# Kernel optimization log

Measured on AMD Instinct MI355X. Metric: run time of the kernel, lower is better.

## Reference

```python
import jax, jax.numpy as jnp
import numpy as np

N = 50000      # nodes / stations
E = 600000     # edges
IN = 16        # in_channels
ED = 8         # edge_dim
HID = 128      # hidden
H = 4          # heads
C = HID // H   # 32 per-head channels
EMB = HID // 2 # station embedding dim
FEAT = HID - EMB
SLOPE = 0.2    # GATv2 LeakyReLU negative slope


def setup_inputs() -> dict:
    key = jax.random.key(0)
    ks = jax.random.split(key, 32)
    r = lambda i, shape, s=0.05: (jax.random.normal(ks[i], shape, jnp.float32) * s)
    inp = {
        "x": jax.random.normal(ks[0], (N, IN), jnp.float32),
        "node_idx": jax.random.randint(ks[1], (N,), 0, N),
        "edge_index": jax.random.randint(ks[2], (2, E), 0, N),
        "edge_attr": jax.random.normal(ks[3], (E, ED), jnp.float32),
        # params
        "emb": r(4, (N, EMB)),
        "W_in": r(5, (IN, FEAT)), "b_in": jnp.zeros((FEAT,), jnp.float32),
        # conv1 (GATv2: lin_l, lin_r, lin_edge, att, out bias)
        "Wl1": r(6, (HID, HID)), "bl1": jnp.zeros((HID,), jnp.float32),
        "Wr1": r(7, (HID, HID)), "br1": jnp.zeros((HID,), jnp.float32),
        "We1": r(8, (ED, HID)),  "be1": jnp.zeros((HID,), jnp.float32),
        "att1": r(9, (H, C)),    "bo1": jnp.zeros((HID,), jnp.float32),
        # conv2
        "Wl2": r(10, (HID, HID)), "bl2": jnp.zeros((HID,), jnp.float32),
        "Wr2": r(11, (HID, HID)), "br2": jnp.zeros((HID,), jnp.float32),
        "We2": r(12, (ED, HID)),  "be2": jnp.zeros((HID,), jnp.float32),
        "att2": r(13, (H, C)),    "bo2": jnp.zeros((HID,), jnp.float32),
        # layer norms
        "g1": jnp.ones((HID,), jnp.float32), "beta1": jnp.zeros((HID,), jnp.float32),
        "g2": jnp.ones((HID,), jnp.float32), "beta2": jnp.zeros((HID,), jnp.float32),
        # output head
        "W_out": r(14, (HID, 1)), "b_out": jnp.zeros((1,), jnp.float32),
    }
    return inp


def _gatv2(x, src, dst, ea, Wl, bl, Wr, br, We, be, att, bo):
    # x: [N,HID] -> per-head projections [N,H,C]
    xl = (x @ Wl + bl).reshape(-1, H, C)   # source transform
    xr = (x @ Wr + br).reshape(-1, H, C)   # target transform
    ee = (ea @ We + be).reshape(-1, H, C)  # edge transform [E,H,C]
    s = jax.nn.leaky_relu(xl[src] + xr[dst] + ee, SLOPE)  # [E,H,C]
    logit = jnp.einsum('ehc,hc->eh', s, att)              # [E,H]
    # segment softmax over destination node
    amax = jax.lax.stop_gradient(jax.ops.segment_max(logit, dst, num_segments=N))
    amax = jnp.where(jnp.isfinite(amax), amax, 0.0)
    ex = jnp.exp(logit - amax[dst])
    den = jax.ops.segment_sum(ex, dst, num_segments=N)
    alpha = ex / den[dst]                                  # [E,H]
    out = jax.ops.segment_sum(xl[src] * alpha[..., None], dst, num_segments=N)
    return out.reshape(-1, HID) + bo


def _ln(x, g, b):
    mu = x.mean(-1, keepdims=True)
    v = ((x - mu) ** 2).mean(-1, keepdims=True)
    return (x - mu) * jax.lax.rsqrt(v + 1e-5) * g + b


def reference(x, node_idx, edge_index, edge_attr, emb, W_in, b_in,
              Wl1, bl1, Wr1, br1, We1, be1, att1, bo1,
              Wl2, bl2, Wr2, br2, We2, be2, att2, bo2,
              g1, beta1, g2, beta2, W_out, b_out):
    src, dst = edge_index[0], edge_index[1]
    feat = jax.nn.relu(x @ W_in + b_in)                       # [N,FEAT]
    z = jnp.concatenate([feat, emb[node_idx]], axis=-1)       # [N,HID]
    h = jax.nn.relu(_gatv2(z, src, dst, edge_attr, Wl1, bl1, Wr1, br1, We1, be1, att1, bo1))
    z = _ln(z + h, g1, beta1)
    h = jax.nn.relu(_gatv2(z, src, dst, edge_attr, Wl2, bl2, Wr2, br2, We2, be2, att2, bo2))
    z = _ln(z + h, g2, beta2)
    return (z @ W_out + b_out).squeeze(-1)                    # [N]
```

## Files before the change

kernel.cpp:

```cpp
#include <hip/hip_runtime.h>
#include <hip/hip_bf16.h>

#define NN 50000
#define NE 600000
#define IND 16
#define EDD 8
#define HIDD 128
#define NH 4
#define CC 32
#define EMBD 64
#define FEATD 64
#define NB_SCAN ((NN + 255) / 256)
#define FILLB ((NE + 255) / 256)
#define BZB (NN / 16)
#define WPB 256
#define PRMF 896

typedef __hip_bfloat16 bf16;
typedef __attribute__((ext_vector_type(8))) short bshort8;
typedef __attribute__((ext_vector_type(4))) float floatx4;
typedef __attribute__((ext_vector_type(2))) float f32x2;

__device__ __forceinline__ unsigned short f2bu(float f) {
    unsigned int u = __float_as_uint(f);
    u += 0x7fffu + ((u >> 16) & 1u);
    return (unsigned short)(u >> 16);
}

#if defined(__has_builtin)
#if __has_builtin(__builtin_amdgcn_fdot2_f32_bf16)
#define HAS_DOT2BF 1
#endif
#endif
#ifndef HAS_DOT2BF
#define HAS_DOT2BF 0
#endif

#if HAS_DOT2BF
typedef __attribute__((ext_vector_type(2))) __bf16 bfx2;
__device__ __forceinline__ float dot2bf(unsigned int a, unsigned int b, float c) {
    return __builtin_amdgcn_fdot2_f32_bf16(__builtin_bit_cast(bfx2, a),
                                           __builtin_bit_cast(bfx2, b), c, false);
}
#else
__device__ __forceinline__ float dot2bf(unsigned int a, unsigned int b, float c) {
    float a0 = __uint_as_float(a << 16), a1 = __uint_as_float(a & 0xffff0000u);
    float b0 = __uint_as_float(b << 16), b1 = __uint_as_float(b & 0xffff0000u);
    return __builtin_fmaf(a1, b1, __builtin_fmaf(a0, b0, c));
}
#endif

template <bool F32>
__device__ __forceinline__ float LD(const void* p, long long i) {
    if constexpr (F32) return ((const float*)p)[i];
    else return __bfloat162float(((const bf16*)p)[i]);
}

__device__ __forceinline__ bool is_f32(const int* cnt) { return *cnt > 8; }

__global__ void k_detinit(const unsigned short* __restrict__ x, int nhalf,
                          int* __restrict__ cnt, int* __restrict__ deg,
                          int* __restrict__ dcnt) {
    if (blockIdx.x == 0) {
        __shared__ int red[256];
        int hits = 0;
        for (int i = threadIdx.x; i < nhalf; i += 256)
            if ((x[i] & 0x7F80u) == 0x7F80u) hits++;
        red[threadIdx.x] = hits;
        __syncthreads();
        for (int o = 128; o; o >>= 1) {
            if (threadIdx.x < o) red[threadIdx.x] += red[threadIdx.x + o];
            __syncthreads();
        }
        if (threadIdx.x == 0) *cnt = red[0];
    } else {
        int gid = (blockIdx.x - 1) * 256 + threadIdx.x;
        if (gid < NN) deg[gid] = 0;
        if (blockIdx.x == 1 && threadIdx.x < 80) dcnt[threadIdx.x] = 0;
    }
}

__global__ void k_hist(const int* __restrict__ ei, int* __restrict__ deg, int* __restrict__ rank) {
    int e = blockIdx.x * blockDim.x + threadIdx.x;
    if (e < NE) rank[e] = atomicAdd(&deg[ei[NE + e]], 1);
}

__global__ void k_scan12(const int* __restrict__ deg, int* __restrict__ off0,
                         int* __restrict__ bsum, int* __restrict__ dcnt,
                         int* __restrict__ dbase, int* __restrict__ rankd) {
    __shared__ int tile[256];
    __shared__ int lh[64];
    __shared__ int lbase[64];
    __shared__ int d2[64];
    __shared__ int ticket;
    int t = threadIdx.x;
    int gid = blockIdx.x * 256 + t;
    if (t < 64) lh[t] = 0;
    __syncthreads();
    int v = (gid < NN) ? deg[gid] : 0;
    int b = 63 - min(v, 63);
    int lr = 0;
    if (gid < NN) lr = atomicAdd(&lh[b], 1);
    tile[t] = v;
    __syncthreads();
    if (t < 64) lbase[t] = lh[t] ? atomicAdd(&dcnt[t], lh[t]) : 0;
    #pragma unroll
    for (int o = 1; o < 256; o <<= 1) {
        int u = (t >= o) ? tile[t - o] : 0;
        __syncthreads();
        tile[t] += u;
        __syncthreads();
    }
    if (gid < NN) {
        off0[gid] = tile[t] - v;
        rankd[gid] = lbase[b] + lr;
    }
    if (t == 255) atomicExch(&bsum[blockIdx.x], tile[255]);
    __syncthreads();
    if (t == 0) ticket = atomicAdd(&dcnt[64], 1);
    __syncthreads();
    if (ticket != NB_SCAN - 1) return;
    int v2 = (t < NB_SCAN) ? atomicAdd(&bsum[t], 0) : 0;
    int dv = (t < 64) ? atomicAdd(&dcnt[t], 0) : 0;
    tile[t] = v2;
    if (t < 64) d2[t] = dv;
    __syncthreads();
    #pragma unroll
    for (int o = 1; o < 256; o <<= 1) {
        int u = (t >= o) ? tile[t - o] : 0;
        __syncthreads();
        tile[t] += u;
        __syncthreads();
    }
    #pragma unroll
    for (int o = 1; o < 64; o <<= 1) {
        int u = (t >= o && t < 64) ? d2[t - o] : 0;
        __syncthreads();
        if (t < 64) d2[t] += u;
        __syncthreads();
    }
    if (t < NB_SCAN) bsum[t] = tile[t] - v2;
    if (t < 64) dbase[t] = d2[t] - dv;
}

template <bool F32>
__device__ void prep_impl(const int* __restrict__ off0, const int* __restrict__ bsum,
                          const int* __restrict__ deg, const int* __restrict__ rankd,
                          const int* __restrict__ dbase, int* __restrict__ perm,
                          int* __restrict__ offF,
                          const int* __restrict__ ei, const int* __restrict__ rank,
                          int* __restrict__ esrc, uint4* __restrict__ ea8, const void* ea,
                          const void* x, const int* __restrict__ node_idx, const void* emb,
                          const void* W_in, const void* b_in, bf16* __restrict__ zb,
                          const void* Wl1, const void* bl1, const void* Wr1, const void* br1,
                          const void* Wl2, const void* bl2, const void* Wr2, const void* br2,
                          bf16* __restrict__ wbT, float* __restrict__ bias,
                          const void* We1, const void* att1, const void* be1, const void* bo1,
                          const void* g1, const void* beta1,
                          const void* We2, const void* att2, const void* be2, const void* bo2,
                          const void* g2, const void* beta2,
                          const void* Wo, const void* bout,
                          unsigned int* __restrict__ wep, float* __restrict__ prm) {
    int b = blockIdx.x;
    int t = threadIdx.x;
    if (b < NB_SCAN) {
        int gid = b * 256 + t;
        if (gid < NN) {
            offF[gid] = off0[gid] + bsum[b];
            int bk = 63 - min(deg[gid], 63);
            perm[dbase[bk] + rankd[gid]] = gid;
        }
        if (gid == 0) offF[NN] = NE;
    } else if (b < NB_SCAN + FILLB) {
        int e = (b - NB_SCAN) * 256 + t;
        if (e >= NE) return;
        if (e < 16) {
            esrc[NE + e] = 0;
            uint4 z; z.x = 0; z.y = 0; z.z = 0; z.w = 0;
            ea8[NE + e] = z;
        }
        int dst = ei[NE + e];
        int slot = off0[dst] + bsum[dst >> 8] + rank[e];
        esrc[slot] = ei[e];
        uint4 v;
        if constexpr (F32) {
            const float4* ef = (const float4*)ea;
            float4 f0 = ef[2 * e], f1 = ef[2 * e + 1];
            v.x = (unsigned int)f2bu(f0.x) | ((unsigned int)f2bu(f0.y) << 16);
            v.y = (unsigned int)f2bu(f0.z) | ((unsigned int)f2bu(f0.w) << 16);
            v.z = (unsigned int)f2bu(f1.x) | ((unsigned int)f2bu(f1.y) << 16);
            v.w = (unsigned int)f2bu(f1.z) | ((unsigned int)f2bu(f1.w) << 16);
        } else {
            v = ((const uint4*)ea)[e];
        }
        ea8[slot] = v;
    } else if (b < NB_SCAN + FILLB + BZB) {
        int nb = (b - NB_SCAN - FILLB) * 16 + (t >> 7) * 8;
        int t7 = t & 127;
        if (t7 < FEATD) {
            float w[IND];
            #pragma unroll
            for (int k = 0; k < IND; k++) w[k] = LD<F32>(W_in, k * FEATD + t7);
            float bi = LD<F32>(b_in, t7);
            #pragma unroll 2
            for (int nd = 0; nd < 8; nd++) {
                int n = nb + nd;
                float acc = bi;
                #pragma unroll
                for (int k = 0; k < IND; k++)
                    acc += LD<F32>(x, (long long)n * IND + k) * w[k];
                zb[n * HIDD + t7] = __float2bfloat16(fmaxf(acc, 0.f));
            }
        } else {
            #pragma unroll 2
            for (int nd = 0; nd < 8; nd++) {
                int n = nb + nd;
                zb[n * HIDD + t7] = __float2bfloat16(
                    LD<F32>(emb, (long long)node_idx[n] * EMBD + (t7 - FEATD)));
            }
        }
    } else if (b < NB_SCAN + FILLB + BZB + WPB) {
        int bid2 = (b - NB_SCAN - FILLB - BZB) * 2 + (t >> 7);
        int layer = bid2 >> 8;
        int n2 = bid2 & 255;
        int t7 = t & 127;
        const void* W = layer ? (n2 < HIDD ? Wl2 : Wr2) : (n2 < HIDD ? Wl1 : Wr1);
        const void* bb = layer ? (n2 < HIDD ? bl2 : br2) : (n2 < HIDD ? bl1 : br1);
        int nn = n2 & (HIDD - 1);
        wbT[(layer * 256 + n2) * HIDD + t7] = __float2bfloat16(LD<F32>(W, t7 * HIDD + nn));
        if (t7 == 0) bias[layer * 256 + n2] = LD<F32>(bb, nn);
    } else {
        int layer = b - (NB_SCAN + FILLB + BZB + WPB);
        const void* We = layer ? We2 : We1;
        const void* att = layer ? att2 : att1;
        const void* be = layer ? be2 : be1;
        const void* bo = layer ? bo2 : bo1;
        const void* g  = layer ? g2 : g1;
        const void* bt = layer ? beta2 : beta1;
        if (t < 128) {
            int lane5 = t >> 2, j = t & 3, c0 = lane5 * 4;
            #pragma unroll
            for (int p = 0; p < 4; p++) {
                unsigned int lo_ = f2bu(LD<F32>(We, (2 * p) * HIDD + c0 + j));
                unsigned int hi_ = f2bu(LD<F32>(We, (2 * p + 1) * HIDD + c0 + j));
                wep[layer * 512 + lane5 * 16 + p * 4 + j] = lo_ | (hi_ << 16);
            }
        } else {
            int t2 = t - 128;
            float* Pp = prm + layer * PRMF;
            Pp[t2]        = LD<F32>(att, t2) * 1.4426950408889634f;
            Pp[128 + t2]  = LD<F32>(be, t2);
            Pp[256 + t2]  = LD<F32>(bo, t2);
            Pp[384 + t2]  = LD<F32>(g, t2);
            Pp[512 + t2]  = LD<F32>(bt, t2);
            if (layer) {
                Pp[640 + t2] = LD<F32>(Wo, t2);
                if (t2 == 0) Pp[768] = LD<F32>(bout, 0);
            }
        }
    }
}
__global__ void k_prep(const int* cnt, const int* off0, const int* bsum, const int* deg,
                       const int* rankd, const int* dbase, int* perm, int* offF,
                       const int* ei, const int* rank, int* esrc, uint4* ea8, const void* ea,
                       const void* x, const int* node_idx, const void* emb,
                       const void* W_in, const void* b_in, bf16* zb,
                       const void* Wl1, const void* bl1, const void* Wr1, const void* br1,
                       const void* Wl2, const void* bl2, const void* Wr2, const void* br2,
                       bf16* wbT, float* bias,
                       const void* We1, const void* att1, const void* be1, const void* bo1,
                       const void* g1, const void* beta1,
                       const void* We2, const void* att2, const void* be2, const void* bo2,
                       const void* g2, const void* beta2,
                       const void* Wo, const void* bout,
                       unsigned int* wep, float* prm) {
    if (is_f32(cnt))
        prep_impl<true>(off0, bsum, deg, rankd, dbase, perm, offF, ei, rank, esrc, ea8, ea,
                        x, node_idx, emb, W_in, b_in, zb, Wl1, bl1, Wr1, br1,
                        Wl2, bl2, Wr2, br2, wbT, bias, We1, att1, be1, bo1, g1, beta1,
                        We2, att2, be2, bo2, g2, beta2, Wo, bout, wep, prm);
    else
        prep_impl<false>(off0, bsum, deg, rankd, dbase, perm, offF, ei, rank, esrc, ea8, ea,
                         x, node_idx, emb, W_in, b_in, zb, Wl1, bl1, Wr1, br1,
                         Wl2, bl2, Wr2, br2, wbT, bias, We1, att1, be1, bo1, g1, beta1,
                         We2, att2, be2, bo2, g2, beta2, Wo, bout, wep, prm);
}

__global__ __launch_bounds__(256) void k_projmm(const bf16* __restrict__ zb,
                                                const bf16* __restrict__ wbT,
                                                const float* __restrict__ bias,
                                                bf16* __restrict__ xl, bf16* __restrict__ xr) {
    int wave = threadIdx.x >> 6, lane = threadIdx.x & 63;
    int n0 = wave * 64;
    int l15 = lane & 15, q = lane >> 4;
    bshort8 afr[4][4];
    #pragma unroll
    for (int j = 0; j < 4; j++)
        #pragma unroll
        for (int s = 0; s < 4; s++)
            afr[j][s] = *(const bshort8*)(wbT + ((n0 + j * 16 + l15) << 7) + s * 32 + q * 8);
    float4 bias4[4];
    #pragma unroll
    for (int j = 0; j < 4; j++) bias4[j] = *(const float4*)(bias + n0 + j * 16 + q * 4);
    bf16* dst = (n0 < HIDD) ? xl : xr;
    int cbase = (n0 & (HIDD - 1)) + q * 4;
    int nodeBase = blockIdx.x * 64;
    #pragma unroll
    for (int mt = 0; mt < 4; mt++) {
        int node = nodeBase + mt * 16 + l15;
        const bf16* brow = zb + (node << 7) + q * 8;
        bshort8 bfrag[4];
        #pragma unroll
        for (int s = 0; s < 4; s++) bfrag[s] = *(const bshort8*)(brow + s * 32);
        floatx4 acc0 = {0.f, 0.f, 0.f, 0.f}, acc1 = acc0, acc2 = acc0, acc3 = acc0;
        #pragma unroll
        for (int s = 0; s < 4; s++) {
            acc0 = __builtin_amdgcn_mfma_f32_16x16x32_bf16(afr[0][s], bfrag[s], acc0, 0, 0, 0);
            acc1 = __builtin_amdgcn_mfma_f32_16x16x32_bf16(afr[1][s], bfrag[s], acc1, 0, 0, 0);
            acc2 = __builtin_amdgcn_mfma_f32_16x16x32_bf16(afr[2][s], bfrag[s], acc2, 0, 0, 0);
            acc3 = __builtin_amdgcn_mfma_f32_16x16x32_bf16(afr[3][s], bfrag[s], acc3, 0, 0, 0);
        }
        if (node < NN) {
            floatx4 accs[4] = {acc0, acc1, acc2, acc3};
            #pragma unroll
            for (int j = 0; j < 4; j++) {
                float4 bv = bias4[j];
                uint2 pk;
                pk.x = (unsigned int)f2bu(accs[j][0] + bv.x) |
                       ((unsigned int)f2bu(accs[j][1] + bv.y) << 16);
                pk.y = (unsigned int)f2bu(accs[j][2] + bv.z) |
                       ((unsigned int)f2bu(accs[j][3] + bv.w) << 16);
                *(uint2*)(dst + (node << 7) + cbase + j * 16) = pk;
            }
        }
    }
}

__device__ __forceinline__ void edge_body(uint4 eu, uint2 xu, const unsigned int (*wp)[4],
                                          const float* base, const f32x2* at2,
                                          float mask, f32x2* acc, float& den) {
    f32x2 xv0, xv1;
    xv0.x = __uint_as_float(xu.x << 16); xv0.y = __uint_as_float(xu.x & 0xffff0000u);
    xv1.x = __uint_as_float(xu.y << 16); xv1.y = __uint_as_float(xu.y & 0xffff0000u);
    f32x2 e01, e23;
    {
        float c0 = base[0];
        c0 = dot2bf(eu.x, wp[0][0], c0);
        c0 = dot2bf(eu.y, wp[1][0], c0);
        c0 = dot2bf(eu.z, wp[2][0], c0);
        c0 = dot2bf(eu.w, wp[3][0], c0);
        float c1 = base[1];
        c1 = dot2bf(eu.x, wp[0][1], c1);
        c1 = dot2bf(eu.y, wp[1][1], c1);
        c1 = dot2bf(eu.z, wp[2][1], c1);
        c1 = dot2bf(eu.w, wp[3][1], c1);
        e01.x = c0; e01.y = c1;
        float c2 = base[2];
        c2 = dot2bf(eu.x, wp[0][2], c2);
        c2 = dot2bf(eu.y, wp[1][2], c2);
        c2 = dot2bf(eu.z, wp[2][2], c2);
        c2 = dot2bf(eu.w, wp[3][2], c2);
        float c3 = base[3];
        c3 = dot2bf(eu.x, wp[0][3], c3);
        c3 = dot2bf(eu.y, wp[1][3], c3);
        c3 = dot2bf(eu.z, wp[2][3], c3);
        c3 = dot2bf(eu.w, wp[3][3], c3);
        e23.x = c2; e23.y = c3;
    }
    f32x2 s0 = xv0 + e01;
    f32x2 s1 = xv1 + e23;
    s0 = __builtin_elementwise_max(s0, s0 * 0.2f);
    s1 = __builtin_elementwise_max(s1, s1 * 0.2f);
    f32x2 lsv = s0 * at2[0] + s1 * at2[1];
    float ls = lsv.x + lsv.y;
    ls += __shfl_xor(ls, 1);
    ls += __shfl_xor(ls, 2);
    ls += __shfl_xor(ls, 4);
    float ex = exp2f(ls) * mask;
    acc[0] += ex * xv0;
    acc[1] += ex * xv1;
    den += ex;
}

template <bool LAST>
__device__ __forceinline__ void gat_impl(const int* __restrict__ perm,
                         const int* __restrict__ off, const int* __restrict__ esrc,
                         const uint4* __restrict__ ea8,
                         const unsigned int* __restrict__ wep,
                         const float* __restrict__ P,
                         const bf16* __restrict__ xl, const bf16* __restrict__ xr,
                         bf16* __restrict__ zb, void* out, bool f32out) {
    int wave = threadIdx.x >> 6;
    int half = (threadIdx.x >> 5) & 1;
    int lane5 = threadIdx.x & 31;
    int n = perm[blockIdx.x * 8 + wave * 2 + half];
    int c0 = lane5 << 2;
    unsigned int wp[4][4];
    {
        const uint4* w4 = (const uint4*)(wep + lane5 * 16);
        uint4 wa = w4[0], wb = w4[1], wc = w4[2], wd = w4[3];
        wp[0][0] = wa.x; wp[0][1] = wa.y; wp[0][2] = wa.z; wp[0][3] = wa.w;
        wp[1][0] = wb.x; wp[1][1] = wb.y; wp[1][2] = wb.z; wp[1][3] = wb.w;
        wp[2][0] = wc.x; wp[2][1] = wc.y; wp[2][2] = wc.z; wp[2][3] = wc.w;
        wp[3][0] = wd.x; wp[3][1] = wd.y; wp[3][2] = wd.z; wp[3][3] = wd.w;
    }
    float4 atv = *(const float4*)(P + c0);
    f32x2 at2[2];
    at2[0].x = atv.x; at2[0].y = atv.y;
    at2[1].x = atv.z; at2[1].y = atv.w;
    float4 bev = *(const float4*)(P + 128 + c0);
    uint2 xru = *(const uint2*)(xr + (n << 7) + c0);
    float base[4];
    base[0] = bev.x + __uint_as_float(xru.x << 16);
    base[1] = bev.y + __uint_as_float(xru.x & 0xffff0000u);
    base[2] = bev.z + __uint_as_float(xru.y << 16);
    base[3] = bev.w + __uint_as_float(xru.y & 0xffff0000u);
    int lo = off[n], hi = off[n + 1];
    f32x2 accA[2] = {{0.f, 0.f}, {0.f, 0.f}}, accB[2] = {{0.f, 0.f}, {0.f, 0.f}};
    float denA = 0.f, denB = 0.f;
    if (lo < hi) {
        int sA = esrc[lo],      sB = esrc[lo + 1];
        int snA = esrc[lo + 2], snB = esrc[lo + 3];
        int s2A = esrc[lo + 4], s2B = esrc[lo + 5];
        int s6A = esrc[lo + 6], s6B = esrc[lo + 7];
        int s8A = esrc[lo + 8], s8B = esrc[lo + 9];
        uint4 eA = ea8[lo],      eB = ea8[lo + 1];
        uint4 enA = ea8[lo + 2], enB = ea8[lo + 3];
        uint4 e2A = ea8[lo + 4], e2B = ea8[lo + 5];
        uint2 xA  = *(const uint2*)(xl + (sA << 7) + c0);
        uint2 xB  = *(const uint2*)(xl + (sB << 7) + c0);
        uint2 xnA = *(const uint2*)(xl + (snA << 7) + c0);
        uint2 xnB = *(const uint2*)(xl + (snB << 7) + c0);
        uint2 x2A = *(const uint2*)(xl + (s2A << 7) + c0);
        uint2 x2B = *(const uint2*)(xl + (s2B << 7) + c0);
        for (int i = lo; i < hi; i += 2) {
            uint2 x3A = *(const uint2*)(xl + (s6A << 7) + c0);
            uint2 x3B = *(const uint2*)(xl + (s6B << 7) + c0);
            uint4 e3A = ea8[i + 6], e3B = ea8[i + 7];
            int s10A = esrc[i + 10], s10B = esrc[i + 11];
            edge_body(eA, xA, wp, base, at2, 1.f, accA, denA);
            float mB = (i + 1 < hi) ? 1.f : 0.f;
            edge_body(eB, xB, wp, base, at2, mB, accB, denB);
            eA = enA; enA = e2A; e2A = e3A;
            eB = enB; enB = e2B; e2B = e3B;
            xA = xnA; xnA = x2A; x2A = x3A;
            xB = xnB; xnB = x2B; x2B = x3B;
            s6A = s8A; s8A = s10A;
            s6B = s8B; s8B = s10B;
        }
        accA[0] += accB[0];
        accA[1] += accB[1];
        denA += denB;
    }
    float inv = (denA > 0.f) ? 1.0f / denA : 0.f;
    uint2 zu = *(const uint2*)(zb + (n << 7) + c0);
    float zv[4];
    zv[0] = __uint_as_float(zu.x << 16);
    zv[1] = __uint_as_float(zu.x & 0xffff0000u);
    zv[2] = __uint_as_float(zu.y << 16);
    zv[3] = __uint_as_float(zu.y & 0xffff0000u);
    float accf[4] = {accA[0].x, accA[0].y, accA[1].x, accA[1].y};
    float4 bo4 = *(const float4*)(P + 256 + c0);
    float bov[4] = {bo4.x, bo4.y, bo4.z, bo4.w};
    float v[4];
    float s = 0.f;
    #pragma unroll
    for (int j = 0; j < 4; j++) {
        float hv = fmaxf(accf[j] * inv + bov[j], 0.f);
        v[j] = zv[j] + hv;
        s += v[j];
    }
    #pragma unroll
    for (int m = 16; m; m >>= 1) s += __shfl_xor(s, m);
    float mu = s * (1.f / HIDD);
    float s2v = 0.f;
    float dv[4];
    #pragma unroll
    for (int j = 0; j < 4; j++) { dv[j] = v[j] - mu; s2v += dv[j] * dv[j]; }
    #pragma unroll
    for (int m = 16; m; m >>= 1) s2v += __shfl_xor(s2v, m);
    float rs = rsqrtf(s2v * (1.f / HIDD) + 1e-5f);
    float4 g4 = *(const float4*)(P + 384 + c0);
    float4 bt4 = *(const float4*)(P + 512 + c0);
    float gv[4] = {g4.x, g4.y, g4.z, g4.w};
    float btv[4] = {bt4.x, bt4.y, bt4.z, bt4.w};
    float o[4];
    #pragma unroll
    for (int j = 0; j < 4; j++)
        o[j] = dv[j] * rs * gv[j] + btv[j];
    if constexpr (!LAST) {
        uint2 pk;
        pk.x = (unsigned int)f2bu(o[0]) | ((unsigned int)f2bu(o[1]) << 16);
        pk.y = (unsigned int)f2bu(o[2]) | ((unsigned int)f2bu(o[3]) << 16);
        *(uint2*)(zb + (n << 7) + c0) = pk;
    } else {
        float4 wo4 = *(const float4*)(P + 640 + c0);
        float wov[4] = {wo4.x, wo4.y, wo4.z, wo4.w};
        float po = 0.f;
        #pragma unroll
        for (int j = 0; j < 4; j++) po += o[j] * wov[j];
        #pragma unroll
        for (int m = 16; m; m >>= 1) po += __shfl_xor(po, m);
        if (lane5 == 0) {
            float r = po + P[768];
            if (f32out) ((float*)out)[n] = r;
            else        ((bf16*)out)[n] = __float2bfloat16(r);
        }
    }
}
__global__ void k_gat(const int* perm, const int* off, const int* esrc,
                      const uint4* ea8, const unsigned int* wep, const float* prm,
                      const bf16* xl, const bf16* xr, bf16* zb) {
    gat_impl<false>(perm, off, esrc, ea8, wep, prm, xl, xr, zb, nullptr, false);
}
__global__ void k_gat_last(const int* cnt, const int* perm, const int* off, const int* esrc,
                           const uint4* ea8, const unsigned int* wep, const float* prm,
                           const bf16* xl, const bf16* xr, bf16* zb, void* out) {
    gat_impl<true>(perm, off, esrc, ea8, wep, prm, xl, xr, zb, out, is_f32(cnt));
}

extern "C" void kernel_launch(void* const* d_in, const int* in_sizes, int n_in,
                              void* d_out, int out_size, void* d_ws, size_t ws_size,
                              hipStream_t stream) {
    const void* x        = d_in[0];
    const int*  node_idx = (const int*)d_in[1];
    const int*  ei       = (const int*)d_in[2];
    const void* ea       = d_in[3];
    const void* emb      = d_in[4];
    const void* W_in     = d_in[5];
    const void* b_in     = d_in[6];
    const void* Wl1 = d_in[7];  const void* bl1 = d_in[8];
    const void* Wr1 = d_in[9];  const void* br1 = d_in[10];
    const void* We1 = d_in[11]; const void* be1 = d_in[12];
    const void* att1 = d_in[13]; const void* bo1 = d_in[14];
    const void* Wl2 = d_in[15]; const void* bl2 = d_in[16];
    const void* Wr2 = d_in[17]; const void* br2 = d_in[18];
    const void* We2 = d_in[19]; const void* be2 = d_in[20];
    const void* att2 = d_in[21]; const void* bo2 = d_in[22];
    const void* g1 = d_in[23]; const void* beta1 = d_in[24];
    const void* g2 = d_in[25]; const void* beta2 = d_in[26];
    const void* W_out = d_in[27]; const void* b_out = d_in[28];

    int*   cnt   = (int*)d_ws;
    uint4* ea8   = (uint4*)((char*)d_ws + 256);
    bf16*  zb    = (bf16*)(ea8 + NE + 16);
    bf16*  xl    = zb + NN * HIDD;
    bf16*  xr    = xl + NN * HIDD;
    bf16*  wbT   = xr + NN * HIDD;
    float* bias  = (float*)(wbT + 2 * 256 * HIDD);
    unsigned int* wep = (unsigned int*)(bias + 512);
    float* prm   = (float*)(wep + 1024);
    int*   off0  = (int*)(prm + 2 * PRMF);
    int*   offF  = off0 + NN + 1;
    int*   deg   = offF + NN + 1;
    int*   rank  = deg + NN;
    int*   rankd = rank + NE;
    int*   perm  = rankd + NN;
    int*   esrc  = perm + NN;
    int*   bsum  = esrc + NE + 16;
    int*   dcnt  = bsum + 256;
    int*   dbase = dcnt + 80;

    int nhalf = in_sizes[0] < 16384 ? in_sizes[0] : 16384;
    k_detinit<<<NB_SCAN + 1, 256, 0, stream>>>((const unsigned short*)x, nhalf, cnt, deg, dcnt);
    k_hist<<<FILLB, 256, 0, stream>>>(ei, deg, rank);
    k_scan12<<<NB_SCAN, 256, 0, stream>>>(deg, off0, bsum, dcnt, dbase, rankd);
    k_prep<<<NB_SCAN + FILLB + BZB + WPB + 2, 256, 0, stream>>>(
        cnt, off0, bsum, deg, rankd, dbase, perm, offF, ei, rank, esrc, ea8, ea,
        x, node_idx, emb, W_in, b_in, zb,
        Wl1, bl1, Wr1, br1, Wl2, bl2, Wr2, br2, wbT, bias,
        We1, att1, be1, bo1, g1, beta1,
        We2, att2, be2, bo2, g2, beta2,
        W_out, b_out, wep, prm);

    k_projmm<<<(NN + 63) / 64, 256, 0, stream>>>(zb, wbT, bias, xl, xr);
    k_gat<<<NN / 8, 256, 0, stream>>>(perm, offF, esrc, ea8, wep, prm, xl, xr, zb);

    k_projmm<<<(NN + 63) / 64, 256, 0, stream>>>(zb, wbT + 256 * HIDD, bias + 256, xl, xr);
    k_gat_last<<<NN / 8, 256, 0, stream>>>(cnt, perm, offF, esrc, ea8, wep + 512, prm + PRMF,
                                           xl, xr, zb, d_out);
}
```

Before: 349.7 us.

## Split CSR edge fill into index scatter plus gather pass fused with projection

The prep kernel now scatters only the original edge id into each CSR slot. A new kernel then gathers the source index and edge attributes per slot, so the attribute writes become coalesced reads-by-index instead of a random scatter. That gather pass shares one launch with the first projection GEMM. The GAT edge loop's prefetch depth for source indices and xl rows is also reduced, trading latency hiding for fewer registers. The extra pass adds one more read and write of esrc.

```diff
diff --git a/kernel.cpp b/kernel.cpp
--- a/kernel.cpp
+++ b/kernel.cpp
@@ -14,6 +14,7 @@
 #define FILLB ((NE + 255) / 256)
 #define BZB (NN / 16)
 #define WPB 256
+#define PJB ((NN + 63) / 64)
 #define PRMF 896
 
 typedef __hip_bfloat16 bf16;
@@ -149,7 +150,7 @@
                           const int* __restrict__ dbase, int* __restrict__ perm,
                           int* __restrict__ offF,
                           const int* __restrict__ ei, const int* __restrict__ rank,
-                          int* __restrict__ esrc, uint4* __restrict__ ea8, const void* ea,
+                          int* __restrict__ esrc,
                           const void* x, const int* __restrict__ node_idx, const void* emb,
                           const void* W_in, const void* b_in, bf16* __restrict__ zb,
                           const void* Wl1, const void* bl1, const void* Wr1, const void* br1,
@@ -174,26 +175,9 @@
     } else if (b < NB_SCAN + FILLB) {
         int e = (b - NB_SCAN) * 256 + t;
         if (e >= NE) return;
-        if (e < 16) {
-            esrc[NE + e] = 0;
-            uint4 z; z.x = 0; z.y = 0; z.z = 0; z.w = 0;
-            ea8[NE + e] = z;
-        }
         int dst = ei[NE + e];
         int slot = off0[dst] + bsum[dst >> 8] + rank[e];
-        esrc[slot] = ei[e];
-        uint4 v;
-        if constexpr (F32) {
-            const float4* ef = (const float4*)ea;
-            float4 f0 = ef[2 * e], f1 = ef[2 * e + 1];
-            v.x = (unsigned int)f2bu(f0.x) | ((unsigned int)f2bu(f0.y) << 16);
-            v.y = (unsigned int)f2bu(f0.z) | ((unsigned int)f2bu(f0.w) << 16);
-            v.z = (unsigned int)f2bu(f1.x) | ((unsigned int)f2bu(f1.y) << 16);
-            v.w = (unsigned int)f2bu(f1.z) | ((unsigned int)f2bu(f1.w) << 16);
-        } else {
-            v = ((const uint4*)ea)[e];
-        }
-        ea8[slot] = v;
+        esrc[slot] = e;
     } else if (b < NB_SCAN + FILLB + BZB) {
         int nb = (b - NB_SCAN - FILLB) * 16 + (t >> 7) * 8;
         int t7 = t & 127;
@@ -262,7 +246,7 @@
 }
 __global__ void k_prep(const int* cnt, const int* off0, const int* bsum, const int* deg,
                        const int* rankd, const int* dbase, int* perm, int* offF,
-                       const int* ei, const int* rank, int* esrc, uint4* ea8, const void* ea,
+                       const int* ei, const int* rank, int* esrc,
                        const void* x, const int* node_idx, const void* emb,
                        const void* W_in, const void* b_in, bf16* zb,
                        const void* Wl1, const void* bl1, const void* Wr1, const void* br1,
@@ -275,21 +259,21 @@
                        const void* Wo, const void* bout,
                        unsigned int* wep, float* prm) {
     if (is_f32(cnt))
-        prep_impl<true>(off0, bsum, deg, rankd, dbase, perm, offF, ei, rank, esrc, ea8, ea,
+        prep_impl<true>(off0, bsum, deg, rankd, dbase, perm, offF, ei, rank, esrc,
                         x, node_idx, emb, W_in, b_in, zb, Wl1, bl1, Wr1, br1,
                         Wl2, bl2, Wr2, br2, wbT, bias, We1, att1, be1, bo1, g1, beta1,
                         We2, att2, be2, bo2, g2, beta2, Wo, bout, wep, prm);
     else
-        prep_impl<false>(off0, bsum, deg, rankd, dbase, perm, offF, ei, rank, esrc, ea8, ea,
+        prep_impl<false>(off0, bsum, deg, rankd, dbase, perm, offF, ei, rank, esrc,
                          x, node_idx, emb, W_in, b_in, zb, Wl1, bl1, Wr1, br1,
                          Wl2, bl2, Wr2, br2, wbT, bias, We1, att1, be1, bo1, g1, beta1,
                          We2, att2, be2, bo2, g2, beta2, Wo, bout, wep, prm);
 }
 
-__global__ __launch_bounds__(256) void k_projmm(const bf16* __restrict__ zb,
-                                                const bf16* __restrict__ wbT,
-                                                const float* __restrict__ bias,
-                                                bf16* __restrict__ xl, bf16* __restrict__ xr) {
+__device__ __forceinline__ void projmm_body(int vb, const bf16* __restrict__ zb,
+                                            const bf16* __restrict__ wbT,
+                                            const float* __restrict__ bias,
+                                            bf16* __restrict__ xl, bf16* __restrict__ xr) {
     int wave = threadIdx.x >> 6, lane = threadIdx.x & 63;
     int n0 = wave * 64;
     int l15 = lane & 15, q = lane >> 4;
@@ -304,7 +288,7 @@
     for (int j = 0; j < 4; j++) bias4[j] = *(const float4*)(bias + n0 + j * 16 + q * 4);
     bf16* dst = (n0 < HIDD) ? xl : xr;
     int cbase = (n0 & (HIDD - 1)) + q * 4;
-    int nodeBase = blockIdx.x * 64;
+    int nodeBase = vb * 64;
     #pragma unroll
     for (int mt = 0; mt < 4; mt++) {
         int node = nodeBase + mt * 16 + l15;
@@ -333,6 +317,49 @@
                 *(uint2*)(dst + (node << 7) + cbase + j * 16) = pk;
             }
         }
+    }
+}
+__global__ __launch_bounds__(256) void k_projmm(const bf16* __restrict__ zb,
+                                                const bf16* __restrict__ wbT,
+                                                const float* __restrict__ bias,
+                                                bf16* __restrict__ xl, bf16* __restrict__ xr) {
+    projmm_body(blockIdx.x, zb, wbT, bias, xl, xr);
+}
+
+template <bool F32>
+__device__ void f2_impl(int* __restrict__ esrc, uint4* __restrict__ ea8,
+                        const int* __restrict__ ei, const void* ea) {
+    int slot = blockIdx.x * 256 + threadIdx.x;
+    if (slot >= NE) return;
+    if (slot < 16) {
+        esrc[NE + slot] = 0;
+        uint4 z; z.x = 0; z.y = 0; z.z = 0; z.w = 0;
+        ea8[NE + slot] = z;
+    }
+    int e = esrc[slot];
+    esrc[slot] = ei[e];
+    uint4 v;
+    if constexpr (F32) {
+        const float4* ef = (const float4*)ea;
+        float4 f0 = ef[2 * e], f1 = ef[2 * e + 1];
+        v.x = (unsigned int)f2bu(f0.x) | ((unsigned int)f2bu(f0.y) << 16);
+        v.y = (unsigned int)f2bu(f0.z) | ((unsigned int)f2bu(f0.w) << 16);
+        v.z = (unsigned int)f2bu(f1.x) | ((unsigned int)f2bu(f1.y) << 16);
+        v.w = (unsigned int)f2bu(f1.z) | ((unsigned int)f2bu(f1.w) << 16);
+    } else {
+        v = ((const uint4*)ea)[e];
+    }
+    ea8[slot] = v;
+}
+__global__ __launch_bounds__(256) void k_f2pm(const int* cnt, int* esrc, uint4* ea8,
+                                              const int* ei, const void* ea,
+                                              const bf16* zb, const bf16* wbT,
+                                              const float* bias, bf16* xl, bf16* xr) {
+    if (blockIdx.x < FILLB) {
+        if (is_f32(cnt)) f2_impl<true>(esrc, ea8, ei, ea);
+        else             f2_impl<false>(esrc, ea8, ei, ea);
+    } else {
+        projmm_body(blockIdx.x - FILLB, zb, wbT, bias, xl, xr);
     }
 }
 
@@ -420,33 +447,28 @@
     float denA = 0.f, denB = 0.f;
     if (lo < hi) {
         int sA = esrc[lo],      sB = esrc[lo + 1];
+        uint4 eA = ea8[lo],     eB = ea8[lo + 1];
         int snA = esrc[lo + 2], snB = esrc[lo + 3];
+        uint4 enA = ea8[lo + 2], enB = ea8[lo + 3];
         int s2A = esrc[lo + 4], s2B = esrc[lo + 5];
-        int s6A = esrc[lo + 6], s6B = esrc[lo + 7];
-        int s8A = esrc[lo + 8], s8B = esrc[lo + 9];
-        uint4 eA = ea8[lo],      eB = ea8[lo + 1];
-        uint4 enA = ea8[lo + 2], enB = ea8[lo + 3];
         uint4 e2A = ea8[lo + 4], e2B = ea8[lo + 5];
-        uint2 xA  = *(const uint2*)(xl + (sA << 7) + c0);
-        uint2 xB  = *(const uint2*)(xl + (sB << 7) + c0);
+        uint2 xA = *(const uint2*)(xl + (sA << 7) + c0);
+        uint2 xB = *(const uint2*)(xl + (sB << 7) + c0);
         uint2 xnA = *(const uint2*)(xl + (snA << 7) + c0);
         uint2 xnB = *(const uint2*)(xl + (snB << 7) + c0);
-        uint2 x2A = *(const uint2*)(xl + (s2A << 7) + c0);
-        uint2 x2B = *(const uint2*)(xl + (s2B << 7) + c0);
         for (int i = lo; i < hi; i += 2) {
-            uint2 x3A = *(const uint2*)(xl + (s6A << 7) + c0);
-            uint2 x3B = *(const uint2*)(xl + (s6B << 7) + c0);
+            uint2 x2A = *(const uint2*)(xl + (s2A << 7) + c0);
+            uint2 x2B = *(const uint2*)(xl + (s2B << 7) + c0);
+            int s3A = esrc[i + 6],  s3B = esrc[i + 7];
             uint4 e3A = ea8[i + 6], e3B = ea8[i + 7];
-            int s10A = esrc[i + 10], s10B = esrc[i + 11];
             edge_body(eA, xA, wp, base, at2, 1.f, accA, denA);
             float mB = (i + 1 < hi) ? 1.f : 0.f;
             edge_body(eB, xB, wp, base, at2, mB, accB, denB);
             eA = enA; enA = e2A; e2A = e3A;
             eB = enB; enB = e2B; e2B = e3B;
-            xA = xnA; xnA = x2A; x2A = x3A;
-            xB = xnB; xnB = x2B; x2B = x3B;
-            s6A = s8A; s8A = s10A;
-            s6B = s8B; s8B = s10B;
+            xA = xnA; xnA = x2A;
+            xB = xnB; xnB = x2B;
+            s2A = s3A; s2B = s3B;
         }
         accA[0] += accB[0];
         accA[1] += accB[1];
@@ -566,17 +588,17 @@
     k_hist<<<FILLB, 256, 0, stream>>>(ei, deg, rank);
     k_scan12<<<NB_SCAN, 256, 0, stream>>>(deg, off0, bsum, dcnt, dbase, rankd);
     k_prep<<<NB_SCAN + FILLB + BZB + WPB + 2, 256, 0, stream>>>(
-        cnt, off0, bsum, deg, rankd, dbase, perm, offF, ei, rank, esrc, ea8, ea,
+        cnt, off0, bsum, deg, rankd, dbase, perm, offF, ei, rank, esrc,
         x, node_idx, emb, W_in, b_in, zb,
         Wl1, bl1, Wr1, br1, Wl2, bl2, Wr2, br2, wbT, bias,
         We1, att1, be1, bo1, g1, beta1,
         We2, att2, be2, bo2, g2, beta2,
         W_out, b_out, wep, prm);
 
-    k_projmm<<<(NN + 63) / 64, 256, 0, stream>>>(zb, wbT, bias, xl, xr);
+    k_f2pm<<<FILLB + PJB, 256, 0, stream>>>(cnt, esrc, ea8, ei, ea, zb, wbT, bias, xl, xr);
     k_gat<<<NN / 8, 256, 0, stream>>>(perm, offF, esrc, ea8, wep, prm, xl, xr, zb);
 
-    k_projmm<<<(NN + 63) / 64, 256, 0, stream>>>(zb, wbT + 256 * HIDD, bias + 256, xl, xr);
+    k_projmm<<<PJB, 256, 0, stream>>>(zb, wbT + 256 * HIDD, bias + 256, xl, xr);
     k_gat_last<<<NN / 8, 256, 0, stream>>>(cnt, perm, offF, esrc, ea8, wep + 512, prm + PRMF,
                                            xl, xr, zb, d_out);
 }
```

Result: no change. 348.2 us (median of 2 runs) (-0.4%).
